# Optimization experiments

Hardware: AMD Instinct MI355X
Metric: run time of the kernel (lower is better)

Reference implementation:

```python
import jax, jax.numpy as jnp
import numpy as np

N, CIN, T = 10000, 64, 64
COUT, K = 64, 3


def setup_inputs() -> dict:
    key = jax.random.key(0)
    k1, k2, k3 = jax.random.split(key, 3)
    x = jax.random.normal(k1, (N, CIN, T), dtype=jnp.float32)
    # torch Conv1d default init: uniform(-1/sqrt(fan_in), 1/sqrt(fan_in))
    bound = 1.0 / np.sqrt(CIN * K)
    weight = jax.random.uniform(k2, (2 * COUT, CIN, K), dtype=jnp.float32, minval=-bound, maxval=bound)
    bias = jax.random.uniform(k3, (2 * COUT,), dtype=jnp.float32, minval=-bound, maxval=bound)
    return {"x": x, "weight": weight, "bias": bias}


def reference(x, weight, bias):
    # Batched 1D conv over time for all nodes at once (equivalent to the
    # per-node loop in the original, since weights are shared).
    # x: [N, Cin, T], weight: [2*Cout, Cin, K] -> y: [N, 2*Cout, T-K+1]
    y = jax.lax.conv_general_dilated(
        x, weight, window_strides=(1,), padding="VALID",
        dimension_numbers=("NCH", "OIH", "NCH"))
    y = y + bias[None, :, None]
    # GLU along channel dim: first half gated by sigmoid of second half
    a, b = jnp.split(y, 2, axis=1)
    return a * jax.nn.sigmoid(b)
```

## Files before the change

kernel.cpp:

```cpp
#include <hip/hip_runtime.h>
#include <hip/hip_bf16.h>

typedef __attribute__((ext_vector_type(8))) short short8;
typedef __attribute__((ext_vector_type(4))) float float4v;

#define NSAMP 10000
#define CIN   64
#define TLEN  64
#define COUT  64
#define TOUT  62

static __device__ __forceinline__ ushort f2bf(float v) {
    unsigned int x = __float_as_uint(v);
    return (ushort)((x + 0x7fffu + ((x >> 16) & 1u)) >> 16);
}

static __device__ __forceinline__ unsigned int cvt_pk_bf16(float a, float b) {
    unsigned int r;
    asm("v_cvt_pk_bf16_f32 %0, %1, %2" : "=v"(r) : "v"(a), "v"(b));
    return r;
}

__global__ void prep_weights(const float* __restrict__ w, ushort* __restrict__ wa) {
    int o = blockIdx.x * blockDim.x + threadIdx.x;
    if (o >= 128 * 192) return;
    int co = o / 192;
    int kk = o - co * 192;
    int k  = kk >> 6;
    int ci = kk & 63;
    wa[o] = f2bf(w[co * 192 + ci * 3 + k]);
}

__global__ __launch_bounds__(256, 4)
void conv_glu(const float* __restrict__ x, const ushort* __restrict__ wa,
              const float* __restrict__ bias, float* __restrict__ out) {
    __shared__ __align__(16) ushort xT[64 * 64];

    const int n   = blockIdx.x;
    const int tid = threadIdx.x;
    const int w   = tid >> 6;
    const int L   = tid & 63;
    const int l   = L & 15;
    const int q   = L >> 4;
    const int h   = w & 1;
    const int nh  = w >> 1;
    const int t0base = nh * 32;

    const float* xs = x + n * (CIN * TLEN);

    {
        const int cig = tid >> 4;
        const int ts  = (tid & 15) * 4;
        const float* p = xs + cig * 4 * TLEN + ts;
        float4v v0 = *(const float4v*)(p);
        float4v v1 = *(const float4v*)(p + TLEN);
        float4v v2 = *(const float4v*)(p + 2 * TLEN);
        float4v v3 = *(const float4v*)(p + 3 * TLEN);
        char* base = (char*)xT;
#pragma unroll
        for (int r = 0; r < 4; ++r) {
            int t = ts + r;
            uint2 val;
            val.x = cvt_pk_bf16(v0[r], v1[r]);
            val.y = cvt_pk_bf16(v2[r], v3[r]);
            *(uint2*)(base + t * 128 + ((cig * 8) ^ ((t & 7) << 4))) = val;
        }
    }
    __syncthreads();

    const ushort* arow[4];
#pragma unroll
    for (int mt = 0; mt < 4; ++mt) {
        int co = 32 * h + 16 * (mt & 1) + 64 * (mt >> 1) + l;
        arow[mt] = wa + co * 192 + q * 8;
    }

    float4v acc[4][2];
#pragma unroll
    for (int mt = 0; mt < 4; ++mt)
#pragma unroll
        for (int nt = 0; nt < 2; ++nt)
            acc[mt][nt] = (float4v){0.f, 0.f, 0.f, 0.f};

#pragma unroll
    for (int kc = 0; kc < 6; ++kc) {
        short8 afr[4];
#pragma unroll
        for (int mt = 0; mt < 4; ++mt)
            afr[mt] = *(const short8*)(arow[mt] + kc * 32);

        const int tap  = kc >> 1;
        const int cib2 = (kc & 1) * 64 + q * 16;
#pragma unroll
        for (int nt = 0; nt < 2; ++nt) {
            int t = t0base + nt * 16 + l + tap;
            if (t > 63) t = 63;
            const short8 bfr = *(const short8*)((const char*)xT + t * 128
                                                + (cib2 ^ ((t & 7) << 4)));
#pragma unroll
            for (int mt = 0; mt < 4; ++mt)
                acc[mt][nt] = __builtin_amdgcn_mfma_f32_16x16x32_bf16(
                    afr[mt], bfr, acc[mt][nt], 0, 0, 0);
        }
    }

#pragma unroll
    for (int p2 = 0; p2 < 2; ++p2) {
#pragma unroll
        for (int nt = 0; nt < 2; ++nt) {
#pragma unroll
            for (int r = 0; r < 4; ++r) {
                int co = 32 * h + 16 * p2 + 4 * q + r;
                int t  = t0base + nt * 16 + l;
                float a = acc[p2][nt][r]     + bias[co];
                float g = acc[p2 + 2][nt][r] + bias[co + 64];
                float sg = 1.0f / (1.0f + __expf(-g));
                if (t < TOUT)
                    out[(n * COUT + co) * TOUT + t] = a * sg;
            }
        }
    }
}

extern "C" void kernel_launch(void* const* d_in, const int* in_sizes, int n_in,
                              void* d_out, int out_size, void* d_ws, size_t ws_size,
                              hipStream_t stream) {
    const float* x    = (const float*)d_in[0];
    const float* wt   = (const float*)d_in[1];
    const float* bias = (const float*)d_in[2];
    ushort*      wa   = (ushort*)d_ws;
    float*       out  = (float*)d_out;

    prep_weights<<<96, 256, 0, stream>>>(wt, wa);
    conv_glu<<<NSAMP, 256, 0, stream>>>(x, wa, bias, out);
}
```

Measured before the change: 361.1 us.

## Split input transpose into prep kernel and use persistent conv kernel with register-resident weights

Adds a prep_x kernel that converts each sample's input to bf16 and transposes it into a time-major layout in workspace. A new persistent conv_glu_xt kernel keeps the weight fragments and bias in registers across samples, folds bias into the accumulator initialisation, and reads B fragments straight from global memory without shared memory or barriers. The goal is to drop the per-block weight reloads and the LDS staging and sync from the main loop. The cost is an extra full pass that writes and rereads about 80 MB of bf16 data, and the original kernel remains as a fallback when the workspace is too small.

```diff
diff --git a/kernel.cpp b/kernel.cpp
--- a/kernel.cpp
+++ b/kernel.cpp
@@ -3,6 +3,8 @@
 
 typedef __attribute__((ext_vector_type(8))) short short8;
 typedef __attribute__((ext_vector_type(4))) float float4v;
+typedef __attribute__((ext_vector_type(2))) unsigned int uint2v;
+typedef __attribute__((ext_vector_type(4))) unsigned int uint4v;
 
 #define NSAMP 10000
 #define CIN   64
@@ -29,6 +31,112 @@
     int k  = kk >> 6;
     int ci = kk & 63;
     wa[o] = f2bf(w[co * 192 + ci * 3 + k]);
+}
+
+__global__ __launch_bounds__(256, 8)
+void prep_x(const float* __restrict__ x, ushort* __restrict__ xt) {
+    __shared__ __align__(16) ushort b[64 * 64];
+    const int n   = blockIdx.x;
+    const int tid = threadIdx.x;
+
+    const int cig = tid >> 4;
+    const int ts  = (tid & 15) * 4;
+    const float* p = x + (long)n * (CIN * TLEN) + cig * 4 * TLEN + ts;
+    float4v v0 = *(const float4v*)(p);
+    float4v v1 = *(const float4v*)(p + TLEN);
+    float4v v2 = *(const float4v*)(p + 2 * TLEN);
+    float4v v3 = *(const float4v*)(p + 3 * TLEN);
+    char* base = (char*)b;
+#pragma unroll
+    for (int r = 0; r < 4; ++r) {
+        int t = ts + r;
+        uint2v val;
+        val.x = cvt_pk_bf16(v0[r], v1[r]);
+        val.y = cvt_pk_bf16(v2[r], v3[r]);
+        *(uint2v*)(base + t * 128 + ((cig * 8) ^ ((t & 7) << 4))) = val;
+    }
+    __syncthreads();
+
+    char* outn = (char*)(xt + (long)n * (TLEN * CIN));
+#pragma unroll
+    for (int i = 0; i < 2; ++i) {
+        int f = i * 256 + tid;
+        int t = f >> 3, c = f & 7;
+        uint4v val = *(const uint4v*)(base + t * 128 + ((c * 16) ^ ((t & 7) << 4)));
+        *(uint4v*)(outn + f * 16) = val;
+    }
+}
+
+__global__ __launch_bounds__(512, 4)
+void conv_glu_xt(const ushort* __restrict__ xt, const ushort* __restrict__ wa,
+                 const float* __restrict__ bias, float* __restrict__ out) {
+    const int tid = threadIdx.x;
+    const int w   = tid >> 6;
+    const int L   = tid & 63;
+    const int l   = L & 15;
+    const int q   = L >> 4;
+    const int h2  = w & 3;
+    const int nh  = w >> 2;
+    const int t0  = nh * 32;
+
+    short8 afr[2][6];
+#pragma unroll
+    for (int mt = 0; mt < 2; ++mt) {
+        int co = 64 * mt + 16 * h2 + l;
+        const short8* wrow = (const short8*)(wa + co * 192);
+#pragma unroll
+        for (int kc = 0; kc < 6; ++kc)
+            afr[mt][kc] = wrow[kc * 4 + q];
+    }
+
+    float bv[4], bg[4];
+#pragma unroll
+    for (int r = 0; r < 4; ++r) {
+        bv[r] = bias[16 * h2 + 4 * q + r];
+        bg[r] = bias[64 + 16 * h2 + 4 * q + r];
+    }
+
+    const int stride = gridDim.x;
+    for (int n = blockIdx.x; n < NSAMP; n += stride) {
+        const char* bbase = (const char*)(xt + (long)n * (TLEN * CIN))
+                            + (t0 + l) * 128 + q * 16;
+
+        float4v acc[2][2];
+#pragma unroll
+        for (int nt = 0; nt < 2; ++nt) {
+            acc[0][nt] = (float4v){bv[0], bv[1], bv[2], bv[3]};
+            acc[1][nt] = (float4v){bg[0], bg[1], bg[2], bg[3]};
+        }
+
+#pragma unroll
+        for (int kc = 0; kc < 6; ++kc) {
+            const int tap = kc >> 1;
+            const int cib = (kc & 1) * 64;
+#pragma unroll
+            for (int nt = 0; nt < 2; ++nt) {
+                const short8 bfr = *(const short8*)(bbase + (nt * 16 + tap) * 128 + cib);
+                acc[0][nt] = __builtin_amdgcn_mfma_f32_16x16x32_bf16(
+                    afr[0][kc], bfr, acc[0][nt], 0, 0, 0);
+                acc[1][nt] = __builtin_amdgcn_mfma_f32_16x16x32_bf16(
+                    afr[1][kc], bfr, acc[1][nt], 0, 0, 0);
+            }
+        }
+
+        char* obase = (char*)out + (long)n * (COUT * TOUT * 4)
+                      + (16 * h2 + 4 * q) * (TOUT * 4) + (t0 + l) * 4;
+#pragma unroll
+        for (int nt = 0; nt < 2; ++nt) {
+            int t = t0 + nt * 16 + l;
+            if (t < TOUT) {
+#pragma unroll
+                for (int r = 0; r < 4; ++r) {
+                    float g  = acc[1][nt][r];
+                    float sg = 1.0f / (1.0f + __expf(-g));
+                    *(float*)(obase + r * (TOUT * 4) + nt * 64) = acc[0][nt][r] * sg;
+                }
+            }
+        }
+    }
 }
 
 __global__ __launch_bounds__(256, 4)
@@ -47,7 +155,6 @@
     const int t0base = nh * 32;
 
     const float* xs = x + n * (CIN * TLEN);
-
     {
         const int cig = tid >> 4;
         const int ts  = (tid & 15) * 4;
@@ -60,10 +167,10 @@
 #pragma unroll
         for (int r = 0; r < 4; ++r) {
             int t = ts + r;
-            uint2 val;
+            uint2v val;
             val.x = cvt_pk_bf16(v0[r], v1[r]);
             val.y = cvt_pk_bf16(v2[r], v3[r]);
-            *(uint2*)(base + t * 128 + ((cig * 8) ^ ((t & 7) << 4))) = val;
+            *(uint2v*)(base + t * 128 + ((cig * 8) ^ ((t & 7) << 4))) = val;
         }
     }
     __syncthreads();
@@ -105,9 +212,9 @@
     }
 
 #pragma unroll
-    for (int p2 = 0; p2 < 2; ++p2) {
-#pragma unroll
-        for (int nt = 0; nt < 2; ++nt) {
+    for (int p2 = 0; p2 < 2; ++p2)
+#pragma unroll
+        for (int nt = 0; nt < 2; ++nt)
 #pragma unroll
             for (int r = 0; r < 4; ++r) {
                 int co = 32 * h + 16 * p2 + 4 * q + r;
@@ -118,8 +225,6 @@
                 if (t < TOUT)
                     out[(n * COUT + co) * TOUT + t] = a * sg;
             }
-        }
-    }
 }
 
 extern "C" void kernel_launch(void* const* d_in, const int* in_sizes, int n_in,
@@ -132,5 +237,13 @@
     float*       out  = (float*)d_out;
 
     prep_weights<<<96, 256, 0, stream>>>(wt, wa);
-    conv_glu<<<NSAMP, 256, 0, stream>>>(x, wa, bias, out);
-}
+
+    const size_t need = 65536 + (size_t)NSAMP * TLEN * CIN * 2 + 4096;
+    if (ws_size >= need) {
+        ushort* xxt = (ushort*)((char*)d_ws + 65536);
+        prep_x<<<NSAMP, 256, 0, stream>>>(x, xxt);
+        conv_glu_xt<<<2048, 512, 0, stream>>>(xxt, wa, bias, out);
+    } else {
+        conv_glu<<<NSAMP, 256, 0, stream>>>(x, wa, bias, out);
+    }
+}
```

New measurement: 408.5 us. 1.13x slower.
